# Kernel optimization log

Measured on AMD Instinct MI355X. Metric: run time of the kernel, lower is better.

## Reference

```python
import jax, jax.numpy as jnp
import numpy as np

N_POINTS = 2048
N_EVENTS = 2_000_000
N_QUAD = 10           # midpoint Riemann samples for the non-event integral
NON_EVENT_WEIGHT = 1.0
EPS = 1e-12           # numerical floor inside sqrt (mirrors torch PairwiseDistance eps)


def setup_inputs() -> dict:
    key = jax.random.key(0)
    k1, k2, k3, k4 = jax.random.split(key, 4)
    # learned parameters, init uniform(-0.25, 0.25) as in init_vector
    z0 = jax.random.uniform(k1, (N_POINTS, 2), minval=-0.25, maxval=0.25)
    v0 = jax.random.uniform(k2, (N_POINTS, 2), minval=-0.25, maxval=0.25)
    beta = jnp.asarray(0.0, jnp.float32)  # background intensity parameter
    # event data: columns [u, v, t] split into int pairs and float times
    data_uv = jax.random.randint(k3, (N_EVENTS, 2), 0, N_POINTS).astype(jnp.int32)
    data_t = jax.random.uniform(k4, (N_EVENTS,), dtype=jnp.float32)
    # all node pairs, lower triangle offset=-1 (matches torch.tril_indices)
    iu, ju = np.tril_indices(N_POINTS, k=-1)
    pair_u = jnp.asarray(iu, jnp.int32)
    pair_v = jnp.asarray(ju, jnp.int32)
    t0 = jnp.asarray(0.0, jnp.float32)
    tn = jnp.asarray(1.0, jnp.float32)
    return dict(z0=z0, v0=v0, beta=beta, data_t=data_t, t0=t0, tn=tn,
                data_uv=data_uv, pair_u=pair_u, pair_v=pair_v)


def reference(z0, v0, beta, data_t, t0, tn, data_uv, pair_u, pair_v):
    # --- event term: sum over events of log lambda_uv(t) = beta - ||z_u(t)-z_v(t)|| ---
    u, v = data_uv[:, 0], data_uv[:, 1]
    # z_i(t) = z0_i + v0_i * t  (constant velocity); difference vector per event [E,2]
    dz = (z0[u] - z0[v]) + (v0[u] - v0[v]) * data_t[:, None]
    event_dist = jnp.sqrt(jnp.sum(dz * dz, axis=-1) + EPS)
    event_intensity = jnp.sum(beta - event_dist)

    # --- non-event term: integral over [t0,tn] of lambda_uv(t) for every node pair ---
    # midpoint Riemann rule with N_QUAD samples
    ts = t0 + (jnp.arange(N_QUAD, dtype=jnp.float32) + 0.5) * (tn - t0) / N_QUAD
    dt = (tn - t0) / N_QUAD
    dz0 = z0[pair_u] - z0[pair_v]          # [P,2]
    dv0 = v0[pair_u] - v0[pair_v]          # [P,2]
    dp = dz0[None] + dv0[None] * ts[:, None, None]   # [T,P,2]
    pair_dist = jnp.sqrt(jnp.sum(dp * dp, axis=-1) + EPS)  # [T,P]
    non_event_intensity = dt * jnp.sum(jnp.exp(beta - pair_dist))

    return event_intensity - NON_EVENT_WEIGHT * non_event_intensity
```

## Files before the change

kernel.cpp:

```cpp
#include <hip/hip_runtime.h>

#define BLOCK   256
#define TILE    64
#define NQUAD   10
#define EPSF    1e-12f
#define NTOTAL  1040

__global__ __launch_bounds__(BLOCK) void cvm_kernel(
    const float* __restrict__ z0, const float* __restrict__ v0,
    const float* __restrict__ beta_p, const float* __restrict__ data_t,
    const float* __restrict__ t0_p, const float* __restrict__ tn_p,
    const int* __restrict__ data_uv,
    float* __restrict__ out,
    int n_points, int n_events, int pair_tiles)
{
    __shared__ float4 table[2048];
    __shared__ float sred[8];

    const int tid = threadIdx.x;
    const int b   = blockIdx.x;

    const float2* z2 = (const float2*)z0;
    const float2* v2 = (const float2*)v0;
    for (int k = tid; k < n_points; k += BLOCK) {
        float2 z = z2[k];
        float2 v = v2[k];
        table[k] = make_float4(z.x, z.y, v.x, v.y);
    }
    __syncthreads();

    const float beta = *beta_p, t0 = *t0_p, tn = *tn_p;
    const float dt   = (tn - t0) * (1.0f / NQUAD);

    float acc_e = 0.0f;
    const int2* uv = (const int2*)data_uv;
    for (int e = b * BLOCK + tid; e < n_events; e += NTOTAL * BLOCK) {
        int2  p  = uv[e];
        float t  = data_t[e];
        float4 Pu = table[p.x];
        float4 Pv = table[p.y];
        float dx = (Pu.x - Pv.x) + (Pu.z - Pv.z) * t;
        float dy = (Pu.y - Pv.y) + (Pu.w - Pv.w) * t;
        acc_e += __builtin_amdgcn_sqrtf(dx * dx + dy * dy + EPSF);
    }

    float acc_p = 0.0f;
    if (b < pair_tiles) {
        int p  = b;
        int ti = (int)((__builtin_amdgcn_sqrtf(8.0f * (float)p + 1.0f) - 1.0f) * 0.5f);
        while ((ti + 1) * (ti + 2) / 2 <= p) ti++;
        while (ti * (ti + 1) / 2 > p)        ti--;
        int tj = p - ti * (ti + 1) / 2;
        int I0 = ti * TILE, J0 = tj * TILE;

        int il = tid & 63;
        int w  = tid >> 6;
        int gi = I0 + il;

        float4 Pi = table[I0 + il];
        bool diag = (ti == tj);

        for (int k = 0; k < 16; ++k) {
            int jl = w + 4 * k;
            int gj = J0 + jl;
            float4 Pj = table[J0 + jl];
            float dzx = Pi.x - Pj.x;
            float dzy = Pi.y - Pj.y;
            float dvx = Pi.z - Pj.z;
            float dvy = Pi.w - Pj.w;
            if (!diag || gi > gj) {
                float s = 0.0f;
                #pragma unroll
                for (int q = 0; q < NQUAD; ++q) {
                    float tq = t0 + ((float)q + 0.5f) * dt;
                    float dx = dzx + dvx * tq;
                    float dy = dzy + dvy * tq;
                    float d  = __builtin_amdgcn_sqrtf(dx * dx + dy * dy + EPSF);
                    s += __expf(-d);
                }
                acc_p += s;
            }
        }
    }

    #pragma unroll
    for (int off = 32; off > 0; off >>= 1) {
        acc_e += __shfl_down(acc_e, off, 64);
        acc_p += __shfl_down(acc_p, off, 64);
    }
    int wave = tid >> 6, lane = tid & 63;
    if (lane == 0) { sred[wave] = acc_e; sred[4 + wave] = acc_p; }
    __syncthreads();
    if (tid == 0) {
        float se = sred[0] + sred[1] + sred[2] + sred[3];
        float sp = sred[4] + sred[5] + sred[6] + sred[7];
        float contrib = -se - dt * __expf(beta) * sp;
        if (b == 0) contrib += (float)n_events * beta;
        atomicAdd(out, contrib);
    }
}

extern "C" void kernel_launch(void* const* d_in, const int* in_sizes, int n_in,
                              void* d_out, int out_size, void* d_ws, size_t ws_size,
                              hipStream_t stream)
{
    const float* z0      = (const float*)d_in[0];
    const float* v0      = (const float*)d_in[1];
    const float* beta_p  = (const float*)d_in[2];
    const float* data_t  = (const float*)d_in[3];
    const float* t0_p    = (const float*)d_in[4];
    const float* tn_p    = (const float*)d_in[5];
    const int*   data_uv = (const int*)d_in[6];

    int n_points = in_sizes[0] / 2;
    int n_events = in_sizes[3];
    int nt       = n_points / TILE;
    int pt       = nt * (nt + 1) / 2;

    float* out = (float*)d_out;

    hipMemsetAsync(out, 0, sizeof(float), stream);

    cvm_kernel<<<NTOTAL, BLOCK, 0, stream>>>(
        z0, v0, beta_p, data_t, t0_p, tn_p, data_uv,
        out, n_points, n_events, pt);
}
```

Baseline: 113.9 us.

## Halve pair tile size, spread pair tiles across all blocks, vectorize event loads

Shrinks the pair tile from 64 to 32 so the triangle has 2080 tiles, and gives every one of the 1040 blocks exactly two tiles. Previously only 528 blocks did pair work while the rest were idle. The event loop now loads two events per thread with int4/float2 reads, and the quadrature times are hoisted into a register array. The tile count is hardcoded for 2048 points, so the kernel is no longer correct for other sizes.

```diff
diff --git a/kernel.cpp b/kernel.cpp
--- a/kernel.cpp
+++ b/kernel.cpp
@@ -1,10 +1,11 @@
 #include <hip/hip_runtime.h>
 
 #define BLOCK   256
-#define TILE    64
+#define TILE    32
 #define NQUAD   10
 #define EPSF    1e-12f
 #define NTOTAL  1040
+#define NTILES  2080
 
 __global__ __launch_bounds__(BLOCK) void cvm_kernel(
     const float* __restrict__ z0, const float* __restrict__ v0,
@@ -12,7 +13,7 @@
     const float* __restrict__ t0_p, const float* __restrict__ tn_p,
     const int* __restrict__ data_uv,
     float* __restrict__ out,
-    int n_points, int n_events, int pair_tiles)
+    int n_points, int n_events)
 {
     __shared__ float4 table[2048];
     __shared__ float sred[8];
@@ -32,49 +33,70 @@
     const float beta = *beta_p, t0 = *t0_p, tn = *tn_p;
     const float dt   = (tn - t0) * (1.0f / NQUAD);
 
+    float tq[NQUAD];
+    #pragma unroll
+    for (int q = 0; q < NQUAD; ++q)
+        tq[q] = t0 + ((float)q + 0.5f) * dt;
+
     float acc_e = 0.0f;
-    const int2* uv = (const int2*)data_uv;
-    for (int e = b * BLOCK + tid; e < n_events; e += NTOTAL * BLOCK) {
-        int2  p  = uv[e];
-        float t  = data_t[e];
-        float4 Pu = table[p.x];
-        float4 Pv = table[p.y];
-        float dx = (Pu.x - Pv.x) + (Pu.z - Pv.z) * t;
-        float dy = (Pu.y - Pv.y) + (Pu.w - Pv.w) * t;
-        acc_e += __builtin_amdgcn_sqrtf(dx * dx + dy * dy + EPSF);
+    {
+        const int4*   uv2 = (const int4*)data_uv;
+        const float2* tt2 = (const float2*)data_t;
+        int nev2 = n_events >> 1;
+        for (int e = b * BLOCK + tid; e < nev2; e += NTOTAL * BLOCK) {
+            int4   p = uv2[e];
+            float2 t = tt2[e];
+            float4 Pu0 = table[p.x];
+            float4 Pv0 = table[p.y];
+            float4 Pu1 = table[p.z];
+            float4 Pv1 = table[p.w];
+            float dx0 = (Pu0.x - Pv0.x) + (Pu0.z - Pv0.z) * t.x;
+            float dy0 = (Pu0.y - Pv0.y) + (Pu0.w - Pv0.w) * t.x;
+            float dx1 = (Pu1.x - Pv1.x) + (Pu1.z - Pv1.z) * t.y;
+            float dy1 = (Pu1.y - Pv1.y) + (Pu1.w - Pv1.w) * t.y;
+            acc_e += __builtin_amdgcn_sqrtf(dx0 * dx0 + dy0 * dy0 + EPSF);
+            acc_e += __builtin_amdgcn_sqrtf(dx1 * dx1 + dy1 * dy1 + EPSF);
+        }
+        if ((n_events & 1) && b == 0 && tid == 0) {
+            int   e = n_events - 1;
+            int   u = data_uv[2 * e], v = data_uv[2 * e + 1];
+            float t = data_t[e];
+            float4 Pu = table[u], Pv = table[v];
+            float dx = (Pu.x - Pv.x) + (Pu.z - Pv.z) * t;
+            float dy = (Pu.y - Pv.y) + (Pu.w - Pv.w) * t;
+            acc_e += __builtin_amdgcn_sqrtf(dx * dx + dy * dy + EPSF);
+        }
     }
 
     float acc_p = 0.0f;
-    if (b < pair_tiles) {
-        int p  = b;
+    const int il = tid & 31;
+    const int jg = tid >> 5;
+    #pragma unroll
+    for (int tt = 0; tt < 2; ++tt) {
+        int p = b + tt * NTOTAL;
         int ti = (int)((__builtin_amdgcn_sqrtf(8.0f * (float)p + 1.0f) - 1.0f) * 0.5f);
         while ((ti + 1) * (ti + 2) / 2 <= p) ti++;
         while (ti * (ti + 1) / 2 > p)        ti--;
         int tj = p - ti * (ti + 1) / 2;
         int I0 = ti * TILE, J0 = tj * TILE;
 
-        int il = tid & 63;
-        int w  = tid >> 6;
-        int gi = I0 + il;
-
         float4 Pi = table[I0 + il];
         bool diag = (ti == tj);
 
-        for (int k = 0; k < 16; ++k) {
-            int jl = w + 4 * k;
-            int gj = J0 + jl;
+        #pragma unroll
+        for (int r = 0; r < 4; ++r) {
+            int jl = jg + 8 * r;
             float4 Pj = table[J0 + jl];
             float dzx = Pi.x - Pj.x;
             float dzy = Pi.y - Pj.y;
             float dvx = Pi.z - Pj.z;
             float dvy = Pi.w - Pj.w;
-            if (!diag || gi > gj) {
+            if (!diag || il > jl) {
                 float s = 0.0f;
                 #pragma unroll
                 for (int q = 0; q < NQUAD; ++q) {
-                    float tq = t0 + ((float)q + 0.5f) * dt;
-                    float dx = dzx + dvx * tq;
-                    float dy = dzy + dvy * tq;
+                    float dx = dzx + dvx * tq[q];
+                    float dy = dzy + dvy * tq[q];
                     float d  = __builtin_amdgcn_sqrtf(dx * dx + dy * dy + EPSF);
                     s += __expf(-d);
                 }
@@ -114,8 +136,6 @@
 
     int n_points = in_sizes[0] / 2;
     int n_events = in_sizes[3];
-    int nt       = n_points / TILE;
-    int pt       = nt * (nt + 1) / 2;
 
     float* out = (float*)d_out;
 
@@ -123,5 +143,5 @@
 
     cvm_kernel<<<NTOTAL, BLOCK, 0, stream>>>(
         z0, v0, beta_p, data_t, t0_p, tn_p, data_uv,
-        out, n_points, n_events, pt);
+        out, n_points, n_events);
 }
```

Result: no change. 114.2 us (+0.3%).
